# Kernel tuning notes

Hardware: AMD Instinct MI355X
Metric: run time of the kernel (lower is better)

## Reference

```python
import jax, jax.numpy as jnp
import numpy as np

# dims
N, T, F, DEMO, H, NHEAD, K, GCN, FFN = 4096, 48, 76, 4, 252, 4, 10, 256, 128
D = H + DEMO          # 256, input dim to graph constructor / clustering / gcn
DK = D // NHEAD       # 64
TAU, MASK_P, LAMBDA_KL, LAMBDA_CL, PHI_INIT, ALPHA = 0.5, 0.1, 1.0, 1.0, 3.0 / N, 1.0


def setup_inputs() -> dict:
    key = jax.random.key(0)
    ks = jax.random.split(key, 16)
    s = 0.02
    return dict(
        x=jax.random.normal(ks[0], (N, T, F), jnp.float32),
        x_demo=jax.random.normal(ks[1], (N, DEMO), jnp.float32),
        sorted_length=jax.random.randint(ks[2], (N,), 1, T + 1),
        mask_edge=jax.random.uniform(ks[3], (N, N), jnp.float32),
        w_ih=jax.random.normal(ks[4], (3 * H, F), jnp.float32) * s,
        w_hh=jax.random.normal(ks[5], (3 * H, H), jnp.float32) * s,
        b_ih=jnp.zeros((3 * H,), jnp.float32),
        b_hh=jnp.zeros((3 * H,), jnp.float32),
        h0=jnp.zeros((H,), jnp.float32),
        wq=jax.random.normal(ks[6], (D, D), jnp.float32) * s,
        bq=jnp.zeros((D,), jnp.float32),
        wk=jax.random.normal(ks[7], (D, D), jnp.float32) * s,
        bk=jnp.zeros((D,), jnp.float32),
        wo=jax.random.normal(ks[8], (NHEAD,), jnp.float32) * s,
        bo=jnp.zeros((), jnp.float32),
        phi=jnp.float32(PHI_INIT),
        centers=jax.random.normal(ks[9], (K, D), jnp.float32),
        gcn_w=jax.random.normal(ks[10], (D, GCN), jnp.float32) * s,
        gcn_b=jnp.zeros((GCN,), jnp.float32),
        ffn_w=jax.random.normal(ks[11], (GCN, FFN), jnp.float32) * s,
        ffn_b=jnp.zeros((FFN,), jnp.float32),
        pre_w=jax.random.normal(ks[12], (GCN, 2), jnp.float32) * s,
        pre_b=jnp.zeros((2,), jnp.float32),
    )


def _forward(x, x_demo, sorted_length, mask_edge, w_ih, w_hh, b_ih, b_hh, h0,
             wq, bq, wk, bk, wo, bo, phi, centers, gcn_w, gcn_b,
             ffn_w, ffn_b, pre_w, pre_b):
    n = x.shape[0]

    # --- GRU over time (torch nn.GRU equations), scan over T ---
    def gru_step(h, xt):
        gi = xt @ w_ih.T + b_ih                     # [N, 3H]
        gh = h @ w_hh.T + b_hh
        ir, iz, inn = jnp.split(gi, 3, axis=-1)
        hr, hz, hn = jnp.split(gh, 3, axis=-1)
        r = jax.nn.sigmoid(ir + hr)
        zg = jax.nn.sigmoid(iz + hz)
        ng = jnp.tanh(inn + r * hn)
        h = (1.0 - zg) * ng + zg * h
        return h, h

    _, outs = jax.lax.scan(gru_step, jnp.broadcast_to(h0, (n, H)), jnp.swapaxes(x, 0, 1))
    idx = jnp.clip(sorted_length - 1, 0, T - 1)
    x_gru = outs[idx, jnp.arange(n)]                # last valid hidden state [N, H]
    x_star = jnp.concatenate([x_gru, x_demo], axis=1)  # [N, D]

    # --- GraphConstructor: multi-head attention adjacency ---
    q = (x_star @ wq.T + bq).reshape(n, NHEAD, DK)
    kk = (x_star @ wk.T + bk).reshape(n, NHEAD, DK)
    scores = jnp.einsum('nhd,mhd->nmh', q, kk) / np.sqrt(DK)  # [N, N, h]
    scores = scores @ wo + bo                                  # Wo: Linear(h, 1)
    attn = jax.nn.softmax(scores, axis=1)
    eye = jnp.eye(n, dtype=x.dtype)
    adj = jnp.where(attn >= phi, 1.0, 0.0) * (1.0 - eye)       # threshold, zero diag

    # --- Clustering: soft assignment around given centers (KMeans fit replaced
    #     by fixed cluster_layer parameter; same soft-assign / KLD math) ---
    d2 = jnp.sum((x_star[:, None, :] - centers[None]) ** 2, axis=-1)  # [N, K]
    qsoft = 1.0 / (1.0 + d2 / ALPHA)
    qsoft = qsoft / jnp.sum(qsoft, axis=1, keepdims=True)
    pdist = qsoft ** 2 / jnp.sum(qsoft, axis=0, keepdims=True)
    pdist = jax.lax.stop_gradient(pdist / jnp.sum(pdist, axis=1, keepdims=True))
    label = jnp.argmax(qsoft, axis=1)
    kl_loss = jnp.mean(jnp.sum(pdist * jnp.log(pdist / (qsoft + 1e-6)), axis=-1))

    # --- GCNConv on dense adjacency (sym-normalized with self loops) ---
    xw = x_star @ gcn_w

    def gcn(a):
        a_hat = a + eye
        dinv = 1.0 / jnp.sqrt(jnp.sum(a_hat, axis=1))
        return (dinv[:, None] * a_hat * dinv[None, :]) @ xw + gcn_b

    z = gcn(adj)
    adj_aug = adj * (mask_edge >= MASK_P).astype(x.dtype)  # DataAug edge mask (bernoulli keep 1-p)
    z_aug = gcn(adj_aug)
    zf = z @ ffn_w + ffn_b
    zfa = z_aug @ ffn_w + ffn_b

    # --- clloss: NxN contrastive loss ---
    def l2n(a):
        return a / jnp.clip(jnp.linalg.norm(a, axis=1, keepdims=True), 1e-12, None)

    zn, zan = l2n(zf), l2n(zfa)
    intra = jnp.exp(zn @ zn.T / TAU)
    inter = jnp.exp(zn @ zan.T / TAU)
    cadj = (label[:, None] == label[None, :]).astype(x.dtype) * (1.0 - eye)
    cadj_new = jnp.where(adj == 1.0, 0.0, cadj)
    positive = jnp.diag(inter) + jnp.sum(intra * adj, axis=1) + jnp.sum(intra * cadj_new, axis=1)
    denom = jnp.sum(intra, axis=1) + jnp.sum(inter, axis=1) - jnp.diag(intra)
    cnt = jnp.sum(adj, axis=1) + jnp.sum(cadj_new, axis=1) + 1.0
    cl_loss = -jnp.sum(jnp.log(positive / denom) / cnt)

    loss = LAMBDA_KL * kl_loss + LAMBDA_CL * cl_loss
    output = z @ pre_w + pre_b
    return output, loss


def reference(x, x_demo, sorted_length, mask_edge, w_ih, w_hh, b_ih, b_hh, h0,
              wq, bq, wk, bk, wo, bo, phi, centers, gcn_w, gcn_b,
              ffn_w, ffn_b, pre_w, pre_b):
    return _forward(x, x_demo, sorted_length, mask_edge, w_ih, w_hh, b_ih, b_hh, h0,
                    wq, bq, wk, bk, wo, bo, phi, centers, gcn_w, gcn_b,
                    ffn_w, ffn_b, pre_w, pre_b)
```

## Files before the change

### kernel.cpp

```cpp
#include <hip/hip_runtime.h>
#include <cstdint>
#include <cstddef>

typedef _Float16 f16;
typedef f16 f16x8 __attribute__((ext_vector_type(8)));
typedef float f32x4 __attribute__((ext_vector_type(4)));

#define MFMA(a,b,c) __builtin_amdgcn_mfma_f32_16x16x32_f16(a,b,c,0,0,0)

__device__ __forceinline__ float sigm(float x){ return 1.f/(1.f+__expf(-x)); }
__device__ __forceinline__ float tanh_f(float x){
  float a = __expf(-2.f*fabsf(x));
  float t = (1.f-a)/(1.f+a);
  return x >= 0.f ? t : -t;
}
__device__ __forceinline__ uint16_t f2bf(float f){
  uint32_t u = __float_as_uint(f);
  return (uint16_t)((u + 0x7fffu + ((u>>16)&1u)) >> 16);
}
__device__ __forceinline__ float bf2f(uint16_t h){
  return __uint_as_float(((uint32_t)h) << 16);
}

__global__ __launch_bounds__(256) void k_prep(
    const float* __restrict__ w_ih, const float* __restrict__ w_hh,
    const float* __restrict__ b_ih, const float* __restrict__ b_hh,
    const int* __restrict__ slen,
    const float* __restrict__ wq, const float* __restrict__ wk,
    const float* __restrict__ gcn_w,
    f16* __restrict__ BgT, f16* __restrict__ wq16, f16* __restrict__ wk16,
    f16* __restrict__ gw16, float* __restrict__ biasc, int* __restrict__ idx)
{
  int id = blockIdx.x*256 + threadIdx.x;
  if (id < 360448){
    int g = id / (256*352); int rem = id % (256*352);
    int j = rem / 352; int k = rem % 352;
    float v = 0.f;
    if (j < 252){
      if (k < 96){
        if (k < 76 && g != 3){
          int row = (g==2) ? (504+j) : (g*252+j);
          v = w_ih[row*76 + k];
        }
      } else {
        int kh = k - 96;
        if (kh < 252 && g != 2){
          int row = (g==3) ? (504+j) : (g*252+j);
          v = w_hh[row*252 + kh];
        }
      }
    }
    BgT[id] = (f16)v;
    return;
  }
  id -= 360448;
  if (id < 65536){ wq16[id] = (f16)wq[id]; return; }
  id -= 65536;
  if (id < 65536){ wk16[id] = (f16)wk[id]; return; }
  id -= 65536;
  if (id < 65536){ int j = id >> 8, d = id & 255; gw16[id] = (f16)gcn_w[d*256 + j]; return; }
  id -= 65536;
  if (id < 1008){
    int g = id / 252, j = id % 252; float v;
    if (g==0) v = b_ih[j] + b_hh[j];
    else if (g==1) v = b_ih[252+j] + b_hh[252+j];
    else if (g==2) v = b_ih[504+j];
    else v = b_hh[504+j];
    biasc[id] = v; return;
  }
  id -= 1008;
  if (id < 4096){
    int s = slen[id] - 1; s = s < 0 ? 0 : (s > 47 ? 47 : s);
    idx[id] = s; return;
  }
}

__global__ __launch_bounds__(256) void k_xt(const float* __restrict__ x,
    f16* __restrict__ x16t)
{
  int id = blockIdx.x*256 + threadIdx.x;
  int c = id % 12; int rem = id / 12;
  int n = rem & 4095; int t = rem >> 12;
  const float* xp = x + ((size_t)n*48 + t)*76;
  f16x8 o;
  #pragma unroll
  for (int e = 0; e < 8; ++e){
    int k = c*8 + e;
    o[e] = (k < 76) ? (f16)xp[k] : (f16)0.f;
  }
  *(f16x8*)(x16t + ((size_t)t*4096 + n)*96 + c*8) = o;
}

__global__ __launch_bounds__(1024, 4) void k_gru_all(
    const f16* __restrict__ x16t, const f16* __restrict__ BgT,
    const float* __restrict__ biasc, const float* __restrict__ h0,
    const int* __restrict__ idxp, float* __restrict__ xstar)
{
  __shared__ f16 hbuf[2][32][256];
  __shared__ int idxl[32];
  int lane = threadIdx.x & 63, w = threadIdx.x >> 6;
  int l16 = lane & 15, lq = lane >> 4;
  int nb = blockIdx.x * 32;

  for (int i = threadIdx.x; i < 32*256; i += 1024){
    int row = i >> 8, c = i & 255;
    int sc = (((c >> 3) ^ (row & 7)) << 3) | (c & 7);
    hbuf[0][row][sc] = (c < 252) ? (f16)h0[c] : (f16)0.f;
  }
  if (threadIdx.x < 32) idxl[threadIdx.x] = idxp[nb + threadIdx.x];

  int j = w*16 + l16;
  bool jv = (j < 252);
  int js = jv ? j : 251;
  float bR = biasc[js], bZ = biasc[252+js], bI = biasc[504+js], bH = biasc[756+js];
  const f16* pR = BgT + (size_t)(0*256 + j)*352 + lq*8;
  const f16* pZ = BgT + (size_t)(1*256 + j)*352 + lq*8;
  const f16* pI = BgT + (size_t)(2*256 + j)*352 + lq*8;
  const f16* pH = BgT + (size_t)(3*256 + j)*352 + lq*8;
  const f16* xp0 = x16t + ((size_t)nb + l16)*96 + lq*8;
  const f16* xp1 = x16t + ((size_t)nb + 16 + l16)*96 + lq*8;

  float hown[2][4];
  #pragma unroll
  for (int mf = 0; mf < 2; ++mf)
  #pragma unroll
  for (int r = 0; r < 4; ++r)
    hown[mf][r] = jv ? h0[js] : 0.f;

  __syncthreads();

  for (int t = 0; t < 48; ++t){
    const f16 (*hin)[256] = hbuf[t & 1];
    f16 (*hout)[256]      = hbuf[(t & 1) ^ 1];
    f32x4 z4 = {0.f,0.f,0.f,0.f};
    f32x4 aR[2] = {z4,z4}, aZ[2] = {z4,z4}, aI[2] = {z4,z4}, aH[2] = {z4,z4};
    size_t xt = (size_t)t*4096*96;

    f16x8 wR[11], wZ[11], wM[11];
    #define LW(u_) do{ \
      wR[u_] = *(const f16x8*)(pR + (u_)*32); \
      wZ[u_] = *(const f16x8*)(pZ + (u_)*32); \
      wM[u_] = ((u_) < 3) ? *(const f16x8*)(pI + (u_)*32) \
                          : *(const f16x8*)(pH + (u_)*32); }while(0)
    LW(0); LW(1);
    #pragma unroll
    for (int u = 0; u < 11; ++u){
      if (u + 2 < 11) LW(u + 2);
      f16x8 a0, a1;
      if (u < 3){
        a0 = *(const f16x8*)(xp0 + xt + u*32);
        a1 = *(const f16x8*)(xp1 + xt + u*32);
      } else {
        int chunk = (u - 3)*4 + lq;
        a0 = *(const f16x8*)(&hin[l16][(chunk ^ (l16 & 7)) << 3]);
        a1 = *(const f16x8*)(&hin[16 + l16][(chunk ^ (l16 & 7)) << 3]);
      }
      aR[0] = MFMA(a0, wR[u], aR[0]);  aR[1] = MFMA(a1, wR[u], aR[1]);
      aZ[0] = MFMA(a0, wZ[u], aZ[0]);  aZ[1] = MFMA(a1, wZ[u], aZ[1]);
      if (u < 3){ aI[0] = MFMA(a0, wM[u], aI[0]);  aI[1] = MFMA(a1, wM[u], aI[1]); }
      else      { aH[0] = MFMA(a0, wM[u], aH[0]);  aH[1] = MFMA(a1, wM[u], aH[1]); }
    }
    #undef LW

    #pragma unroll
    for (int mf = 0; mf < 2; ++mf)
    #pragma unroll
    for (int r = 0; r < 4; ++r){
      int row = mf*16 + lq*4 + r;
      float rr = sigm(aR[mf][r] + bR);
      float zz = sigm(aZ[mf][r] + bZ);
      float ng = tanh_f(aI[mf][r] + bI + rr*(aH[mf][r] + bH));
      float hnew = (1.f - zz)*ng + zz*hown[mf][r];
      hnew = jv ? hnew : 0.f;
      hown[mf][r] = hnew;
      int sc = (((j >> 3) ^ (row & 7)) << 3) | (j & 7);
      hout[row][sc] = (f16)hnew;
      if (jv && idxl[row] == t) xstar[((size_t)(nb + row) << 8) + j] = hnew;
    }
    __syncthreads();
  }
}

__global__ __launch_bounds__(256) void k_xstar(const float* __restrict__ x_demo,
    float* __restrict__ xs32, f16* __restrict__ xs16)
{
  int id = blockIdx.x*256 + threadIdx.x;
  int n = id >> 8, c = id & 255;
  float v;
  if (c < 252) v = xs32[id];
  else v = x_demo[n*4 + (c - 252)];
  xs32[id] = v;
  xs16[id] = (f16)v;
}

template<int MODE>
__global__ __launch_bounds__(256) void k_proj(const f16* __restrict__ xs16,
    const f16* __restrict__ w16, const float* __restrict__ bias,
    const float* __restrict__ wo, f16* __restrict__ out16)
{
  int lane = threadIdx.x & 63, wv = threadIdx.x >> 6;
  int l16 = lane & 15, lq = lane >> 4;
  int nb = blockIdx.x * 64;
  int ocol = blockIdx.y*64 + wv*16 + l16;
  f32x4 z4 = {0.f,0.f,0.f,0.f};
  f32x4 acc[4] = {z4,z4,z4,z4};
  #pragma unroll
  for (int ks = 0; ks < 8; ++ks){
    f16x8 b = *(const f16x8*)(w16 + (size_t)ocol*256 + ks*32 + lq*8);
    #pragma unroll
    for (int mi = 0; mi < 4; ++mi){
      f16x8 a = *(const f16x8*)(xs16 + (size_t)(nb + mi*16 + l16)*256 + ks*32 + lq*8);
      acc[mi] = MFMA(a, b, acc[mi]);
    }
  }
  float badd = bias[ocol];
  float scale = (MODE == 0) ? wo[ocol >> 6]*0.125f : 1.f;
  #pragma unroll
  for (int mi = 0; mi < 4; ++mi)
  #pragma unroll
  for (int r = 0; r < 4; ++r){
    int n = nb + mi*16 + lq*4 + r;
    float v = acc[mi][r] + badd;
    if (MODE == 0) v *= scale;
    out16[(size_t)n*256 + ocol] = (f16)v;
  }
}

__global__ __launch_bounds__(256) void k_scores(const f16* __restrict__ qf,
    const f16* __restrict__ kf, uint16_t* __restrict__ sco)
{
  int lane = threadIdx.x & 63, w = threadIdx.x >> 6;
  int l16 = lane & 15, lq = lane >> 4;
  int mh = w >> 1, jh = w & 1;
  int nb = blockIdx.x*128 + mh*64;
  int mb = blockIdx.y*128 + jh*64;
  f32x4 z4 = {0.f,0.f,0.f,0.f};
  f32x4 acc[4][4];
  #pragma unroll
  for (int i = 0; i < 4; ++i)
  #pragma unroll
  for (int j = 0; j < 4; ++j) acc[i][j] = z4;
  #pragma unroll
  for (int ks = 0; ks < 8; ++ks){
    f16x8 a[4], b[4];
    #pragma unroll
    for (int i = 0; i < 4; ++i){
      a[i] = *(const f16x8*)(qf + (size_t)(nb + i*16 + l16)*256 + ks*32 + lq*8);
      b[i] = *(const f16x8*)(kf + (size_t)(mb + i*16 + l16)*256 + ks*32 + lq*8);
    }
    #pragma unroll
    for (int mi = 0; mi < 4; ++mi)
    #pragma unroll
    for (int jf = 0; jf < 4; ++jf)
      acc[mi][jf] = MFMA(a[mi], b[jf], acc[mi][jf]);
  }
  #pragma unroll
  for (int mi = 0; mi < 4; ++mi)
  #pragma unroll
  for (int jf = 0; jf < 4; ++jf)
  #pragma unroll
  for (int r = 0; r < 4; ++r){
    int n = nb + mi*16 + lq*4 + r;
    int m = mb + jf*16 + l16;
    sco[((size_t)n << 12) + m] = f2bf(acc[mi][jf][r]);
  }
}

__global__ __launch_bounds__(256) void k_adj(const uint16_t* __restrict__ sco,
    const float* __restrict__ mask_edge, const float* __restrict__ phip,
    uint8_t* __restrict__ flags, float* __restrict__ sadj,
    float* __restrict__ dinv, float* __restrict__ dinva)
{
  int n = blockIdx.x;
  int lane = threadIdx.x & 63, wv = threadIdx.x >> 6;
  const uint16_t* row = sco + ((size_t)n << 12);
  int base = threadIdx.x * 16;
  const uint4* p = (const uint4*)(row + base);
  uint4 w0 = p[0], w1 = p[1];
  uint32_t ws_[8] = {w0.x,w0.y,w0.z,w0.w,w1.x,w1.y,w1.z,w1.w};
  float v[16];
  #pragma unroll
  for (int i = 0; i < 8; ++i){
    v[2*i]   = bf2f((uint16_t)(ws_[i] & 0xffffu));
    v[2*i+1] = bf2f((uint16_t)(ws_[i] >> 16));
  }
  float mx = v[0];
  #pragma unroll
  for (int i = 1; i < 16; ++i) mx = fmaxf(mx, v[i]);
  #pragma unroll
  for (int o = 32; o >= 1; o >>= 1) mx = fmaxf(mx, __shfl_xor(mx, o));
  __shared__ float redA[4], redB[4], redC[4], redD[4];
  if (lane == 0) redA[wv] = mx;
  __syncthreads();
  mx = fmaxf(fmaxf(redA[0], redA[1]), fmaxf(redA[2], redA[3]));
  float s = 0.f;
  #pragma unroll
  for (int i = 0; i < 16; ++i) s += __expf(v[i] - mx);
  #pragma unroll
  for (int o = 32; o >= 1; o >>= 1) s += __shfl_xor(s, o);
  if (lane == 0) redB[wv] = s;
  __syncthreads();
  float rs = 1.f / (redB[0] + redB[1] + redB[2] + redB[3]);
  float phi = phip[0];
  uint32_t by[16]; int c0 = 0, c1 = 0;
  #pragma unroll
  for (int e = 0; e < 16; ++e){
    float a = __expf(v[e] - mx) * rs;
    int col = base + e;
    uint32_t b = (a >= phi && col != n) ? 1u : 0u;
    if (b){ if (mask_edge[((size_t)n << 12) + col] >= 0.1f) b |= 2u; }
    by[e] = b;
    c0 += (int)(b & 1u);
    c1 += (int)(b >> 1);
  }
  uint4 pk;
  pk.x = by[0]  | (by[1]  << 8) | (by[2]  << 16) | (by[3]  << 24);
  pk.y = by[4]  | (by[5]  << 8) | (by[6]  << 16) | (by[7]  << 24);
  pk.z = by[8]  | (by[9]  << 8) | (by[10] << 16) | (by[11] << 24);
  pk.w = by[12] | (by[13] << 8) | (by[14] << 16) | (by[15] << 24);
  *(uint4*)(flags + ((size_t)n << 12) + base) = pk;
  float f0 = (float)c0, f1 = (float)c1;
  #pragma unroll
  for (int o = 32; o >= 1; o >>= 1){ f0 += __shfl_xor(f0, o); f1 += __shfl_xor(f1, o); }
  if (lane == 0){ redC[wv] = f0; redD[wv] = f1; }
  __syncthreads();
  if (threadIdx.x == 0){
    float d0 = redC[0]+redC[1]+redC[2]+redC[3];
    float d1 = redD[0]+redD[1]+redD[2]+redD[3];
    sadj[n] = d0;
    dinv[n]  = rsqrtf(1.f + d0);
    dinva[n] = rsqrtf(1.f + d1);
  }
}

__global__ __launch_bounds__(256) void k_xw_y(const f16* __restrict__ xs16,
    const f16* __restrict__ gw16, const float* __restrict__ dinv,
    const float* __restrict__ dinva, f16* __restrict__ y16, f16* __restrict__ ya16)
{
  int lane = threadIdx.x & 63, wv = threadIdx.x >> 6;
  int l16 = lane & 15, lq = lane >> 4;
  int nb = blockIdx.x * 64;
  int jcol = blockIdx.y*64 + wv*16 + l16;
  f32x4 z4 = {0.f,0.f,0.f,0.f};
  f32x4 acc[4] = {z4,z4,z4,z4};
  #pragma unroll
  for (int ks = 0; ks < 8; ++ks){
    f16x8 b = *(const f16x8*)(gw16 + (size_t)jcol*256 + ks*32 + lq*8);
    #pragma unroll
    for (int mi = 0; mi < 4; ++mi){
      f16x8 a = *(const f16x8*)(xs16 + (size_t)(nb + mi*16 + l16)*256 + ks*32 + lq*8);
      acc[mi] = MFMA(a, b, acc[mi]);
    }
  }
  #pragma unroll
  for (int mi = 0; mi < 4; ++mi)
  #pragma unroll
  for (int r = 0; r < 4; ++r){
    int n = nb + mi*16 + lq*4 + r;
    float v = acc[mi][r];
    y16[(size_t)n*256 + jcol]  = (f16)(dinv[n]*v);
    ya16[(size_t)n*256 + jcol] = (f16)(dinva[n]*v);
  }
}

__global__ __launch_bounds__(256) void k_zgather(const uint8_t* __restrict__ flags,
    const f16* __restrict__ y16, const f16* __restrict__ ya16,
    const float* __restrict__ dinv, const float* __restrict__ dinva,
    const float* __restrict__ gcn_b, float* __restrict__ z32, float* __restrict__ za32)
{
  int n = blockIdx.x;
  int lane = threadIdx.x & 63, wv = threadIdx.x >> 6;
  uint4 w = ((const uint4*)(flags + ((size_t)n << 12)))[threadIdx.x];
  uint32_t m0[4] = {w.x & 0x01010101u, w.y & 0x01010101u, w.z & 0x01010101u, w.w & 0x01010101u};
  uint32_t m1[4] = {w.x & 0x02020202u, w.y & 0x02020202u, w.z & 0x02020202u, w.w & 0x02020202u};
  int c0 = __popc(m0[0]) + __popc(m0[1]) + __popc(m0[2]) + __popc(m0[3]);
  int c1 = __popc(m1[0]) + __popc(m1[1]) + __popc(m1[2]) + __popc(m1[3]);
  int v0 = c0, v1 = c1;
  #pragma unroll
  for (int o = 1; o < 64; o <<= 1){
    int u0 = __shfl_up(v0, o), u1 = __shfl_up(v1, o);
    if (lane >= o){ v0 += u0; v1 += u1; }
  }
  __shared__ int wsum0[4], wsum1[4];
  if (lane == 63){ wsum0[wv] = v0; wsum1[wv] = v1; }
  __syncthreads();
  int pos0 = v0 - c0, pos1 = v1 - c1;
  #pragma unroll
  for (int i = 0; i < 4; ++i) if (i < wv){ pos0 += wsum0[i]; pos1 += wsum1[i]; }
  int tot0 = wsum0[0]+wsum0[1]+wsum0[2]+wsum0[3];
  int tot1 = wsum1[0]+wsum1[1]+wsum1[2]+wsum1[3];
  __shared__ uint16_t list0[4096];
  __shared__ uint16_t list1[4096];
  int cbase = threadIdx.x * 16;
  #pragma unroll
  for (int q = 0; q < 4; ++q){
    uint32_t m = m0[q];
    while (m){
      int b = __ffs(m) - 1;
      list0[pos0++] = (uint16_t)(cbase + q*4 + (b >> 3));
      m &= m - 1;
    }
    m = m1[q];
    while (m){
      int b = __ffs(m) - 1;
      list1[pos1++] = (uint16_t)(cbase + q*4 + (b >> 3));
      m &= m - 1;
    }
  }
  __syncthreads();
  int j = threadIdx.x;
  float acc0 = (float)y16[((size_t)n << 8) + j];
  float acc1 = (float)ya16[((size_t)n << 8) + j];
  for (int i = 0; i < tot0; ++i) acc0 += (float)y16[((size_t)list0[i] << 8) + j];
  for (int i = 0; i < tot1; ++i) acc1 += (float)ya16[((size_t)list1[i] << 8) + j];
  z32[((size_t)n << 8) + j]  = dinv[n]*acc0 + gcn_b[j];
  za32[((size_t)n << 8) + j] = dinva[n]*acc1 + gcn_b[j];
}

__global__ __launch_bounds__(256) void k_cluster(const float* __restrict__ xs32,
    const float* __restrict__ centers, float* __restrict__ qsoft,
    int* __restrict__ labels, float* __restrict__ colsum)
{
  int nb = blockIdx.x * 16;
  __shared__ float xs[16][256];
  __shared__ float ct[2560];
  __shared__ float d2s[16][10];
  __shared__ float qs[16][10];
  for (int i = threadIdx.x; i < 16*256; i += 256) xs[i >> 8][i & 255] = xs32[(size_t)nb*256 + i];
  for (int i = threadIdx.x; i < 2560; i += 256){ int k = i >> 8, d = i & 255; ct[d*10 + k] = centers[i]; }
  __syncthreads();
  if (threadIdx.x < 160){
    int r = threadIdx.x / 10, k = threadIdx.x % 10;
    float s = 0.f;
    for (int d = 0; d < 256; ++d){ float df = xs[r][d] - ct[d*10 + k]; s += df*df; }
    d2s[r][k] = s;
  }
  __syncthreads();
  if (threadIdx.x < 16){
    int r = threadIdx.x;
    float un[10]; float tot = 0.f;
    #pragma unroll
    for (int k = 0; k < 10; ++k){ un[k] = 1.f/(1.f + d2s[r][k]); tot += un[k]; }
    float inv = 1.f / tot;
    int best = 0; float bm = un[0];
    #pragma unroll
    for (int k = 1; k < 10; ++k){ if (un[k] > bm){ bm = un[k]; best = k; } }
    labels[nb + r] = best;
    #pragma unroll
    for (int k = 0; k < 10; ++k){ float q = un[k]*inv; qs[r][k] = q; qsoft[(size_t)(nb + r)*10 + k] = q; }
  }
  __syncthreads();
  if (threadIdx.x < 10){
    int k = threadIdx.x; float s = 0.f;
    #pragma unroll
    for (int r = 0; r < 16; ++r) s += qs[r][k];
    atomicAdd(&colsum[k], s);
  }
}

__global__ __launch_bounds__(256) void k_kl(const float* __restrict__ qsoft,
    const float* __restrict__ colsum, float* __restrict__ klsum)
{
  int n = blockIdx.x*256 + threadIdx.x;
  float p[10]; float s = 0.f;
  #pragma unroll
  for (int k = 0; k < 10; ++k){
    float q = qsoft[(size_t)n*10 + k];
    float pu = q*q/colsum[k];
    p[k] = pu; s += pu;
  }
  float inv = 1.f/s; float kl = 0.f;
  #pragma unroll
  for (int k = 0; k < 10; ++k){
    float pk = p[k]*inv;
    float q = qsoft[(size_t)n*10 + k];
    kl += pk*__logf(pk/(q + 1e-6f));
  }
  int lane = threadIdx.x & 63, wv = threadIdx.x >> 6;
  #pragma unroll
  for (int o = 32; o >= 1; o >>= 1) kl += __shfl_xor(kl, o);
  __shared__ float red[4];
  if (lane == 0) red[wv] = kl;
  __syncthreads();
  if (threadIdx.x == 0) atomicAdd(klsum, red[0]+red[1]+red[2]+red[3]);
}

__global__ __launch_bounds__(128) void k_ffn(const float* __restrict__ z32,
    const float* __restrict__ za32, const float* __restrict__ ffn_w,
    const float* __restrict__ ffn_b, f16* __restrict__ zn16, f16* __restrict__ zan16)
{
  int n = blockIdx.x; int aug = blockIdx.y;
  const float* z = (aug ? za32 : z32) + ((size_t)n << 8);
  __shared__ float zr[256];
  zr[threadIdx.x] = z[threadIdx.x];
  zr[threadIdx.x + 128] = z[threadIdx.x + 128];
  __syncthreads();
  int j = threadIdx.x;
  float acc = ffn_b[j];
  #pragma unroll 8
  for (int d = 0; d < 256; ++d) acc += zr[d]*ffn_w[d*128 + j];
  float ss = acc*acc;
  int lane = threadIdx.x & 63, wv = threadIdx.x >> 6;
  #pragma unroll
  for (int o = 32; o >= 1; o >>= 1) ss += __shfl_xor(ss, o);
  __shared__ float sred[2];
  if (lane == 0) sred[wv] = ss;
  __syncthreads();
  float tot = sred[0] + sred[1];
  float rn = 1.f / fmaxf(sqrtf(tot), 1e-12f);
  (aug ? zan16 : zn16)[((size_t)n << 7) + j] = (f16)(acc*rn);
}

__global__ __launch_bounds__(256) void k_closs(const f16* __restrict__ zn,
    const f16* __restrict__ zan, const uint8_t* __restrict__ flags,
    const int* __restrict__ labels,
    float* __restrict__ rs1, float* __restrict__ rs2, float* __restrict__ rsA,
    float* __restrict__ rsC, float* __restrict__ rcC, float* __restrict__ rdI,
    float* __restrict__ rdi)
{
  int lane = threadIdx.x & 63;
  int ji = threadIdx.x >> 6;
  int l16 = lane & 15, lq = lane >> 4;
  int nb = blockIdx.x * 32;
  int mstart = blockIdx.y * 512;
  f16x8 A[2][4];
  #pragma unroll
  for (int mi = 0; mi < 2; ++mi)
  #pragma unroll
  for (int ks = 0; ks < 4; ++ks)
    A[mi][ks] = *(const f16x8*)(zn + (size_t)(nb + mi*16 + l16)*128 + ks*32 + lq*8);
  int labn[8];
  #pragma unroll
  for (int i = 0; i < 8; ++i) labn[i] = labels[nb + (i >> 2)*16 + lq*4 + (i & 3)];
  float a1[8]={}, a2[8]={}, aA[8]={}, aC[8]={}, aCc[8]={}, adI[8]={}, adi[8]={};
  for (int tile = 0; tile < 8; ++tile){
    int mcol = mstart + tile*64 + ji*16 + l16;
    uint8_t flv[8];
    #pragma unroll
    for (int i = 0; i < 8; ++i){
      int n = nb + (i >> 2)*16 + lq*4 + (i & 3);
      flv[i] = flags[((size_t)n << 12) + mcol];
    }
    int labm = labels[mcol];
    f32x4 z4 = {0.f,0.f,0.f,0.f};
    f32x4 acc1[2] = {z4, z4};
    f32x4 acc2[2] = {z4, z4};
    #pragma unroll
    for (int ks = 0; ks < 4; ++ks){
      f16x8 b1 = *(const f16x8*)(zn  + (size_t)mcol*128 + ks*32 + lq*8);
      f16x8 b2 = *(const f16x8*)(zan + (size_t)mcol*128 + ks*32 + lq*8);
      #pragma unroll
      for (int mi = 0; mi < 2; ++mi){
        acc1[mi] = MFMA(A[mi][ks], b1, acc1[mi]);
        acc2[mi] = MFMA(A[mi][ks], b2, acc2[mi]);
      }
    }
    #pragma unroll
    for (int mi = 0; mi < 2; ++mi)
    #pragma unroll
    for (int r = 0; r < 4; ++r){
      int i8 = mi*4 + r;
      int n = nb + mi*16 + lq*4 + r;
      float e1 = __expf(2.f*acc1[mi][r]);
      float e2 = __expf(2.f*acc2[mi][r]);
      uint8_t fl = flv[i8];
      a1[i8] += e1; a2[i8] += e2;
      bool adjb = (fl & 1);
      if (adjb) aA[i8] += e1;
      if (!adjb && labn[i8] == labm && n != mcol){ aC[i8] += e1; aCc[i8] += 1.f; }
      if (n == mcol){ adI[i8] += e2; adi[i8] += e1; }
    }
  }
  #pragma unroll
  for (int i = 0; i < 8; ++i){
    #pragma unroll
    for (int o = 1; o < 16; o <<= 1){
      a1[i]  += __shfl_xor(a1[i], o);  a2[i]  += __shfl_xor(a2[i], o);
      aA[i]  += __shfl_xor(aA[i], o);  aC[i]  += __shfl_xor(aC[i], o);
      aCc[i] += __shfl_xor(aCc[i], o); adI[i] += __shfl_xor(adI[i], o);
      adi[i] += __shfl_xor(adi[i], o);
    }
  }
  if (l16 == 0){
    #pragma unroll
    for (int i = 0; i < 8; ++i){
      int n = nb + (i >> 2)*16 + lq*4 + (i & 3);
      atomicAdd(&rs1[n], a1[i]);  atomicAdd(&rs2[n], a2[i]);
      atomicAdd(&rsA[n], aA[i]);  atomicAdd(&rsC[n], aC[i]);
      atomicAdd(&rcC[n], aCc[i]); atomicAdd(&rdI[n], adI[i]);
      atomicAdd(&rdi[n], adi[i]);
    }
  }
}

__global__ __launch_bounds__(256) void k_clfinal(const float* __restrict__ rs1,
    const float* __restrict__ rs2, const float* __restrict__ rsA,
    const float* __restrict__ rsC, const float* __restrict__ rcC,
    const float* __restrict__ rdI, const float* __restrict__ rdi,
    const float* __restrict__ sadj, float* __restrict__ clsum)
{
  int n = blockIdx.x*256 + threadIdx.x;
  float pos = rdI[n] + rsA[n] + rsC[n];
  float den = rs1[n] + rs2[n] - rdi[n];
  float cnt = sadj[n] + rcC[n] + 1.f;
  float v = __logf(pos/den)/cnt;
  int lane = threadIdx.x & 63, wv = threadIdx.x >> 6;
  #pragma unroll
  for (int o = 32; o >= 1; o >>= 1) v += __shfl_xor(v, o);
  __shared__ float red[4];
  if (lane == 0) red[wv] = v;
  __syncthreads();
  if (threadIdx.x == 0) atomicAdd(clsum, red[0]+red[1]+red[2]+red[3]);
}

__global__ void k_loss(const float* __restrict__ scal, float* __restrict__ out){
  out[8192] = scal[0]*(1.f/4096.f) - scal[1];
}

__global__ __launch_bounds__(256) void k_outhead(const float* __restrict__ z32,
    const float* __restrict__ pre_w, const float* __restrict__ pre_b,
    float* __restrict__ out)
{
  int lane = threadIdx.x & 63, wv = threadIdx.x >> 6;
  int n = blockIdx.x*4 + wv;
  float4 zv = *(const float4*)(z32 + ((size_t)n << 8) + lane*4);
  float4 w0 = *(const float4*)(pre_w + lane*8);
  float4 w1 = *(const float4*)(pre_w + lane*8 + 4);
  float c0 = zv.x*w0.x + zv.y*w0.z + zv.z*w1.x + zv.w*w1.z;
  float c1 = zv.x*w0.y + zv.y*w0.w + zv.z*w1.y + zv.w*w1.w;
  #pragma unroll
  for (int o = 32; o >= 1; o >>= 1){ c0 += __shfl_xor(c0, o); c1 += __shfl_xor(c1, o); }
  if (lane == 0){
    out[(size_t)n*2]     = c0 + pre_b[0];
    out[(size_t)n*2 + 1] = c1 + pre_b[1];
  }
}

extern "C" void kernel_launch(void* const* d_in, const int* in_sizes, int n_in,
                              void* d_out, int out_size, void* d_ws, size_t ws_size,
                              hipStream_t stream)
{
  const float* x         = (const float*)d_in[0];
  const float* x_demo    = (const float*)d_in[1];
  const int*   slen      = (const int*)d_in[2];
  const float* mask_edge = (const float*)d_in[3];
  const float* w_ih      = (const float*)d_in[4];
  const float* w_hh      = (const float*)d_in[5];
  const float* b_ih      = (const float*)d_in[6];
  const float* b_hh      = (const float*)d_in[7];
  const float* h0        = (const float*)d_in[8];
  const float* wq        = (const float*)d_in[9];
  const float* bq        = (const float*)d_in[10];
  const float* wk        = (const float*)d_in[11];
  const float* bk        = (const float*)d_in[12];
  const float* wo        = (const float*)d_in[13];
  const float* phi       = (const float*)d_in[15];
  const float* centers   = (const float*)d_in[16];
  const float* gcn_w     = (const float*)d_in[17];
  const float* gcn_b     = (const float*)d_in[18];
  const float* ffn_w     = (const float*)d_in[19];
  const float* ffn_b     = (const float*)d_in[20];
  const float* pre_w     = (const float*)d_in[21];
  const float* pre_b     = (const float*)d_in[22];
  float* out = (float*)d_out;

  size_t off = 0;
  char* base = (char*)d_ws;
  auto take = [&](size_t bytes)->void*{
    void* p = base + off;
    off += (bytes + 255) & ~(size_t)255;
    return p;
  };
  f16*   BgT    = (f16*)take((size_t)4*256*352*2);
  f16*   wq16   = (f16*)take((size_t)65536*2);
  f16*   wk16   = (f16*)take((size_t)65536*2);
  f16*   gw16   = (f16*)take((size_t)65536*2);
  float* biasc  = (float*)take(1008*4);
  int*   idx    = (int*)take(4096*4);
  float* xs32   = (float*)take((size_t)4096*256*4);
  f16*   xs16   = (f16*)take((size_t)4096*256*2);
  f16*   qf16   = (f16*)take((size_t)4096*256*2);
  f16*   kf16   = (f16*)take((size_t)4096*256*2);
  uint16_t* sco = (uint16_t*)take((size_t)4096*4096*2);
  uint8_t* flags= (uint8_t*)take((size_t)4096*4096);
  float* sadj   = (float*)take(4096*4);
  float* dinv   = (float*)take(4096*4);
  float* dinva  = (float*)take(4096*4);
  f16*   y16    = (f16*)take((size_t)4096*256*2);
  f16*   ya16   = (f16*)take((size_t)4096*256*2);
  float* z32    = (float*)take((size_t)4096*256*4);
  float* za32   = (float*)take((size_t)4096*256*4);
  f16*   zn16   = (f16*)take((size_t)4096*128*2);
  f16*   zan16  = (f16*)take((size_t)4096*128*2);
  float* qsoft  = (float*)take((size_t)4096*10*4);
  int*   labels = (int*)take(4096*4);
  float* colsum = (float*)take(64);
  float* scal   = (float*)take(64);
  float* rsbuf  = (float*)take((size_t)7*4096*4);
  float* rs1 = rsbuf,        *rs2 = rsbuf + 4096, *rsA = rsbuf + 2*4096;
  float* rsC = rsbuf + 3*4096, *rcC = rsbuf + 4*4096;
  float* rdI = rsbuf + 5*4096, *rdi = rsbuf + 6*4096;

  f16* x16t = (f16*)sco;

  hipMemsetAsync(colsum, 0, 64, stream);
  hipMemsetAsync(scal, 0, 64, stream);
  hipMemsetAsync(rsbuf, 0, (size_t)7*4096*4, stream);

  k_prep<<<2196, 256, 0, stream>>>(w_ih, w_hh, b_ih, b_hh, slen, wq, wk, gcn_w,
                                   BgT, wq16, wk16, gw16, biasc, idx);
  k_xt<<<9216, 256, 0, stream>>>(x, x16t);
  k_gru_all<<<128, 1024, 0, stream>>>(x16t, BgT, biasc, h0, idx, xs32);
  k_xstar<<<4096, 256, 0, stream>>>(x_demo, xs32, xs16);
  k_proj<0><<<dim3(64, 4), 256, 0, stream>>>(xs16, wq16, bq, wo, qf16);
  k_proj<1><<<dim3(64, 4), 256, 0, stream>>>(xs16, wk16, bk, wo, kf16);
  k_scores<<<dim3(32, 32), 256, 0, stream>>>(qf16, kf16, sco);
  k_adj<<<4096, 256, 0, stream>>>(sco, mask_edge, phi, flags, sadj, dinv, dinva);
  k_xw_y<<<dim3(64, 4), 256, 0, stream>>>(xs16, gw16, dinv, dinva, y16, ya16);
  k_zgather<<<4096, 256, 0, stream>>>(flags, y16, ya16, dinv, dinva, gcn_b, z32, za32);
  k_cluster<<<256, 256, 0, stream>>>(xs32, centers, qsoft, labels, colsum);
  k_kl<<<16, 256, 0, stream>>>(qsoft, colsum, &scal[0]);
  k_ffn<<<dim3(4096, 2), 128, 0, stream>>>(z32, za32, ffn_w, ffn_b, zn16, zan16);
  k_closs<<<dim3(128, 8), 256, 0, stream>>>(zn16, zan16, flags, labels,
                                            rs1, rs2, rsA, rsC, rcC, rdI, rdi);
  k_clfinal<<<16, 256, 0, stream>>>(rs1, rs2, rsA, rsC, rcC, rdI, rdi, sadj, &scal[1]);
  k_loss<<<1, 1, 0, stream>>>(scal, out);
  k_outhead<<<1024, 256, 0, stream>>>(z32, pre_w, pre_b, out);

  (void)in_sizes; (void)n_in; (void)out_size; (void)ws_size;
}
```

Before: 999.3 us.

## Pipeline GRU weight loads, fuse xstar fp16 write into GRU, prefetch closs flags

The GRU step's weight-fragment loads become a four-deep rotating register pipeline, with asm pins so the compiler keeps each load ahead of its MFMAs. The GRU kernel now writes the fp16 copy of the final hidden state directly, and the old full-size xstar pass is reduced to a small kernel that only fills the demographic columns. The contrastive-loss kernel prefetches the next tile's flags and labels while the current tile computes. The pins and prefetch buffers raise register pressure in kernels already near their limits.

```diff
diff --git a/kernel.cpp b/kernel.cpp
--- a/kernel.cpp
+++ b/kernel.cpp
@@ -94,7 +94,8 @@
 __global__ __launch_bounds__(1024, 4) void k_gru_all(
     const f16* __restrict__ x16t, const f16* __restrict__ BgT,
     const float* __restrict__ biasc, const float* __restrict__ h0,
-    const int* __restrict__ idxp, float* __restrict__ xstar)
+    const int* __restrict__ idxp, float* __restrict__ xstar,
+    f16* __restrict__ xs16)
 {
   __shared__ f16 hbuf[2][32][256];
   __shared__ int idxl[32];
@@ -136,31 +137,46 @@
     f32x4 aR[2] = {z4,z4}, aZ[2] = {z4,z4}, aI[2] = {z4,z4}, aH[2] = {z4,z4};
     size_t xt = (size_t)t*4096*96;
 
-    f16x8 wR[11], wZ[11], wM[11];
-    #define LW(u_) do{ \
-      wR[u_] = *(const f16x8*)(pR + (u_)*32); \
-      wZ[u_] = *(const f16x8*)(pZ + (u_)*32); \
-      wM[u_] = ((u_) < 3) ? *(const f16x8*)(pI + (u_)*32) \
-                          : *(const f16x8*)(pH + (u_)*32); }while(0)
-    LW(0); LW(1);
-    #pragma unroll
-    for (int u = 0; u < 11; ++u){
-      if (u + 2 < 11) LW(u + 2);
-      f16x8 a0, a1;
-      if (u < 3){
-        a0 = *(const f16x8*)(xp0 + xt + u*32);
-        a1 = *(const f16x8*)(xp1 + xt + u*32);
-      } else {
-        int chunk = (u - 3)*4 + lq;
-        a0 = *(const f16x8*)(&hin[l16][(chunk ^ (l16 & 7)) << 3]);
-        a1 = *(const f16x8*)(&hin[16 + l16][(chunk ^ (l16 & 7)) << 3]);
-      }
-      aR[0] = MFMA(a0, wR[u], aR[0]);  aR[1] = MFMA(a1, wR[u], aR[1]);
-      aZ[0] = MFMA(a0, wZ[u], aZ[0]);  aZ[1] = MFMA(a1, wZ[u], aZ[1]);
-      if (u < 3){ aI[0] = MFMA(a0, wM[u], aI[0]);  aI[1] = MFMA(a1, wM[u], aI[1]); }
-      else      { aH[0] = MFMA(a0, wM[u], aH[0]);  aH[1] = MFMA(a1, wM[u], aH[1]); }
-    }
-    #undef LW
+    f16x8 R0,Z0,M0, R1,Z1,M1, R2,Z2,M2, R3,Z3,M3;
+#define PIN(s) asm volatile("" :: "v"(*(const f32x4*)&R##s), \
+                                  "v"(*(const f32x4*)&Z##s), \
+                                  "v"(*(const f32x4*)&M##s))
+#define LW(s,u) do{ \
+      R##s = *(const f16x8*)(pR + (u)*32); \
+      Z##s = *(const f16x8*)(pZ + (u)*32); \
+      M##s = *(const f16x8*)((((u) < 3) ? pI : pH) + (u)*32); \
+      PIN(s); }while(0)
+#define STEP(s,u) do{ \
+      f16x8 a0, a1; \
+      if ((u) < 3){ \
+        a0 = *(const f16x8*)(xp0 + xt + (u)*32); \
+        a1 = *(const f16x8*)(xp1 + xt + (u)*32); \
+      } else { \
+        int chunk = ((u) - 3)*4 + lq; \
+        a0 = *(const f16x8*)(&hin[l16][(chunk ^ (l16 & 7)) << 3]); \
+        a1 = *(const f16x8*)(&hin[16 + l16][(chunk ^ (l16 & 7)) << 3]); \
+      } \
+      aR[0] = MFMA(a0, R##s, aR[0]);  aR[1] = MFMA(a1, R##s, aR[1]); \
+      aZ[0] = MFMA(a0, Z##s, aZ[0]);  aZ[1] = MFMA(a1, Z##s, aZ[1]); \
+      if ((u) < 3){ aI[0] = MFMA(a0, M##s, aI[0]);  aI[1] = MFMA(a1, M##s, aI[1]); } \
+      else        { aH[0] = MFMA(a0, M##s, aH[0]);  aH[1] = MFMA(a1, M##s, aH[1]); } \
+    }while(0)
+
+    LW(0,0); LW(1,1); LW(2,2); LW(3,3);
+    STEP(0,0);   LW(0,4);
+    STEP(1,1);   LW(1,5);
+    STEP(2,2);   LW(2,6);
+    STEP(3,3);   LW(3,7);
+    STEP(0,4);   LW(0,8);
+    STEP(1,5);   LW(1,9);
+    STEP(2,6);   LW(2,10);
+    STEP(3,7);
+    STEP(0,8);
+    STEP(1,9);
+    STEP(2,10);
+#undef LW
+#undef STEP
+#undef PIN
 
     #pragma unroll
     for (int mf = 0; mf < 2; ++mf)
@@ -175,22 +191,23 @@
       hown[mf][r] = hnew;
       int sc = (((j >> 3) ^ (row & 7)) << 3) | (j & 7);
       hout[row][sc] = (f16)hnew;
-      if (jv && idxl[row] == t) xstar[((size_t)(nb + row) << 8) + j] = hnew;
+      if (jv && idxl[row] == t){
+        xstar[((size_t)(nb + row) << 8) + j] = hnew;
+        xs16[((size_t)(nb + row) << 8) + j] = (f16)hnew;
+      }
     }
     __syncthreads();
   }
 }
 
-__global__ __launch_bounds__(256) void k_xstar(const float* __restrict__ x_demo,
+__global__ __launch_bounds__(256) void k_xdemo(const float* __restrict__ x_demo,
     float* __restrict__ xs32, f16* __restrict__ xs16)
 {
   int id = blockIdx.x*256 + threadIdx.x;
-  int n = id >> 8, c = id & 255;
-  float v;
-  if (c < 252) v = xs32[id];
-  else v = x_demo[n*4 + (c - 252)];
-  xs32[id] = v;
-  xs16[id] = (f16)v;
+  int n = id >> 2, c = id & 3;
+  float v = x_demo[id];
+  xs32[((size_t)n << 8) + 252 + c] = v;
+  xs16[((size_t)n << 8) + 252 + c] = (f16)v;
 }
 
 template<int MODE>
@@ -533,15 +550,29 @@
   #pragma unroll
   for (int i = 0; i < 8; ++i) labn[i] = labels[nb + (i >> 2)*16 + lq*4 + (i & 3)];
   float a1[8]={}, a2[8]={}, aA[8]={}, aC[8]={}, aCc[8]={}, adI[8]={}, adi[8]={};
+  uint8_t fA[8]; int labA;
+  {
+    int mcol0 = mstart + ji*16 + l16;
+    #pragma unroll
+    for (int i = 0; i < 8; ++i){
+      int n = nb + (i >> 2)*16 + lq*4 + (i & 3);
+      fA[i] = flags[((size_t)n << 12) + mcol0];
+    }
+    labA = labels[mcol0];
+  }
+  #pragma unroll
   for (int tile = 0; tile < 8; ++tile){
     int mcol = mstart + tile*64 + ji*16 + l16;
-    uint8_t flv[8];
-    #pragma unroll
-    for (int i = 0; i < 8; ++i){
-      int n = nb + (i >> 2)*16 + lq*4 + (i & 3);
-      flv[i] = flags[((size_t)n << 12) + mcol];
-    }
-    int labm = labels[mcol];
+    uint8_t fB[8]; int labB = 0;
+    if (tile < 7){
+      int mn = mcol + 64;
+      #pragma unroll
+      for (int i = 0; i < 8; ++i){
+        int n = nb + (i >> 2)*16 + lq*4 + (i & 3);
+        fB[i] = flags[((size_t)n << 12) + mn];
+      }
+      labB = labels[mn];
+    }
     f32x4 z4 = {0.f,0.f,0.f,0.f};
     f32x4 acc1[2] = {z4, z4};
     f32x4 acc2[2] = {z4, z4};
@@ -563,12 +594,17 @@
       int n = nb + mi*16 + lq*4 + r;
       float e1 = __expf(2.f*acc1[mi][r]);
       float e2 = __expf(2.f*acc2[mi][r]);
-      uint8_t fl = flv[i8];
+      uint8_t fl = fA[i8];
       a1[i8] += e1; a2[i8] += e2;
       bool adjb = (fl & 1);
       if (adjb) aA[i8] += e1;
-      if (!adjb && labn[i8] == labm && n != mcol){ aC[i8] += e1; aCc[i8] += 1.f; }
+      if (!adjb && labn[i8] == labA && n != mcol){ aC[i8] += e1; aCc[i8] += 1.f; }
       if (n == mcol){ adI[i8] += e2; adi[i8] += e1; }
+    }
+    if (tile < 7){
+      #pragma unroll
+      for (int i = 0; i < 8; ++i) fA[i] = fB[i];
+      labA = labB;
     }
   }
   #pragma unroll
@@ -710,8 +746,8 @@
   k_prep<<<2196, 256, 0, stream>>>(w_ih, w_hh, b_ih, b_hh, slen, wq, wk, gcn_w,
                                    BgT, wq16, wk16, gw16, biasc, idx);
   k_xt<<<9216, 256, 0, stream>>>(x, x16t);
-  k_gru_all<<<128, 1024, 0, stream>>>(x16t, BgT, biasc, h0, idx, xs32);
-  k_xstar<<<4096, 256, 0, stream>>>(x_demo, xs32, xs16);
+  k_xdemo<<<64, 256, 0, stream>>>(x_demo, xs32, xs16);
+  k_gru_all<<<128, 1024, 0, stream>>>(x16t, BgT, biasc, h0, idx, xs32, xs16);
   k_proj<0><<<dim3(64, 4), 256, 0, stream>>>(xs16, wq16, bq, wo, qf16);
   k_proj<1><<<dim3(64, 4), 256, 0, stream>>>(xs16, wk16, bk, wo, kf16);
   k_scores<<<dim3(32, 32), 256, 0, stream>>>(qf16, kf16, sco);
```

Measured after the change: 874.7 us. 1.14x faster.
